# Performance work log

Measured on AMD Instinct MI355X. Metric: run time of the kernel, lower is better.

Reference implementation:

```python
import jax, jax.numpy as jnp
import numpy as np

N_CLASSES = 4
N_FEATURES = 13
N_HIDDEN = 13
N_STEPS = 100
FORGET_BIAS = 1.0


def setup_inputs() -> dict:
    key = jax.random.key(0)
    ks = jax.random.split(key, 10)
    B = 32768
    return {
        "x_input": jax.random.normal(ks[0], (B, N_STEPS, N_FEATURES), dtype=jnp.float32),
        # input projection (tf.random.normal mean=0.5 in original; values irrelevant for correctness test)
        "w_hidden": jax.random.normal(ks[1], (N_FEATURES, N_HIDDEN), dtype=jnp.float32) * 0.5 + 0.5,
        "b_hidden": jax.random.normal(ks[2], (N_HIDDEN,), dtype=jnp.float32) * 0.5 + 0.5,
        # BasicLSTMCell params: kernel [input_dim + hidden, 4*hidden], gate order (i, j, f, o)
        "lstm0_kernel": jax.random.normal(ks[3], (N_HIDDEN + N_HIDDEN, 4 * N_HIDDEN), dtype=jnp.float32) * 0.2,
        "lstm0_bias": jnp.zeros((4 * N_HIDDEN,), dtype=jnp.float32),
        "lstm1_kernel": jax.random.normal(ks[4], (N_HIDDEN + N_HIDDEN, 4 * N_HIDDEN), dtype=jnp.float32) * 0.2,
        "lstm1_bias": jnp.zeros((4 * N_HIDDEN,), dtype=jnp.float32),
        "w_output": jax.random.normal(ks[5], (N_HIDDEN, N_CLASSES), dtype=jnp.float32) * 0.5 + 0.5,
        "b_output": jax.random.normal(ks[6], (N_CLASSES,), dtype=jnp.float32) * 0.5 + 0.5,
    }


def _lstm_cell(x, c, h, kernel, bias):
    # BasicLSTMCell: z = [x; h] @ W + b, split -> i, j, f, o
    z = jnp.concatenate([x, h], axis=-1) @ kernel + bias
    i, j, f, o = jnp.split(z, 4, axis=-1)
    c_new = c * jax.nn.sigmoid(f + FORGET_BIAS) + jax.nn.sigmoid(i) * jnp.tanh(j)
    h_new = jnp.tanh(c_new) * jax.nn.sigmoid(o)
    return c_new, h_new


def reference(x_input, w_hidden, b_hidden, lstm0_kernel, lstm0_bias,
              lstm1_kernel, lstm1_bias, w_output, b_output):
    B = x_input.shape[0]
    # input projection + relu, batched over all timesteps: [B,T,F] -> [T,B,H]
    hidden = jax.nn.relu(jnp.einsum('btf,fh->bth', x_input, w_hidden) + b_hidden)
    hidden = jnp.transpose(hidden, (1, 0, 2))  # [T, B, H]

    zeros = jnp.zeros((B, N_HIDDEN), dtype=x_input.dtype)
    init = (zeros, zeros, zeros, zeros)  # (c0, h0, c1, h1)

    def step(carry, x_t):
        c0, h0, c1, h1 = carry
        c0, h0 = _lstm_cell(x_t, c0, h0, lstm0_kernel, lstm0_bias)
        c1, h1 = _lstm_cell(h0, c1, h1, lstm1_kernel, lstm1_bias)
        return (c0, h0, c1, h1), None

    (c0, h0, c1, h1), _ = jax.lax.scan(step, init, hidden)
    # last output of top LSTM layer -> output projection
    return h1 @ w_output + b_output
```

## Files before the change

### kernel.cpp

```cpp
#include <hip/hip_runtime.h>
#include <cstdint>

typedef __bf16          bf16x8 __attribute__((ext_vector_type(8)));
typedef float           f32x4  __attribute__((ext_vector_type(4)));
typedef unsigned short  u16x8  __attribute__((ext_vector_type(8)));

#define MFMA16(a,b,c) __builtin_amdgcn_mfma_f32_16x16x32_bf16((a),(b),(c),0,0,0)

__device__ __forceinline__ float rcpf(float x) { return __builtin_amdgcn_rcpf(x); }
__device__ __forceinline__ float ex2(float x)  { return __builtin_amdgcn_exp2f(x); }

__device__ __forceinline__ void split2(float v, unsigned short& hi, unsigned short& lo) {
    unsigned u = __builtin_bit_cast(unsigned, v);
    hi = (unsigned short)(u >> 16);
    float rem = v - __builtin_bit_cast(float, u & 0xffff0000u);
    lo = (unsigned short)(__builtin_bit_cast(unsigned, rem) >> 16);
}
__device__ __forceinline__ __bf16 bfbits(unsigned short b) { return __builtin_bit_cast(__bf16, b); }


constexpr float KL = 1.4426950408889634f;

__global__ __launch_bounds__(256, 4)
void lstm_fused(const float* __restrict__ x,
                const float* __restrict__ w_hidden,
                const float* __restrict__ b_hidden,
                const float* __restrict__ k0,
                const float* __restrict__ b0,
                const float* __restrict__ k1,
                const float* __restrict__ b1,
                const float* __restrict__ w_out,
                const float* __restrict__ b_out,
                float* __restrict__ out)
{
    __shared__ __attribute__((aligned(16))) unsigned short xh_s[2][2][2][384];
    __shared__ __attribute__((aligned(16))) unsigned short h0_s[2][2][2][384];
    __shared__ __attribute__((aligned(16))) unsigned short h1_s[2][2][384];

    const int lane = threadIdx.x & 63;
    const int wv   = threadIdx.x >> 6;
    const int grp  = wv >> 1;
    const int role = wv & 1;
    const int col  = lane & 15;
    const int q    = lane >> 4;
    const int qh   = q & 1;
    const int s0   = (blockIdx.x * 2 + grp) * 16;

    {
        unsigned short* a0 = &xh_s[0][0][0][0];
        unsigned short* a1 = &h0_s[0][0][0][0];
        for (int idx = threadIdx.x; idx < 3072; idx += 256) {
            unsigned short v = ((idx % 24) == 13 && ((idx / 384) & 1) == 0)
                             ? (unsigned short)0x3F80 : (unsigned short)0;
            a0[idx] = v; a1[idx] = v;
        }
        unsigned short* a2 = &h1_s[0][0][0];
        for (int idx = threadIdx.x; idx < 1536; idx += 256) {
            unsigned short v = ((idx % 24) == 13 && ((idx / 384) & 1) == 0)
                             ? (unsigned short)0x3F80 : (unsigned short)0;
            a2[idx] = v;
        }
    }

    const float* kp = role ? k1 : k0;
    const float* bb = role ? b1 : b0;
    bf16x8 Kh[4], Kl[4];
    #pragma unroll
    for (int g = 0; g < 4; ++g) {
        bf16x8 hv{}, lv{};
        #pragma unroll
        for (int j = 0; j < 8; ++j) {
            int k = 8 * q + j;
            float w = 0.f;
            if (col < 13) {
                if (k < 13)                 w = kp[k * 52 + 13 * g + col];
                else if (k == 13)           w = bb[13 * g + col] + (g == 2 ? 1.f : 0.f);
                else if (k >= 16 && k < 29) w = kp[(13 + k - 16) * 52 + 13 * g + col];
            }
            unsigned short h_, l_;
            split2(w, h_, l_);
            hv[j] = bfbits(h_); lv[j] = bfbits(l_);
        }
        Kh[g] = hv; Kl[g] = lv;
    }

    bf16x8 Ph{}, Pl{};
    if (role) {
        #pragma unroll
        for (int j = 0; j < 8; ++j) {
            int k = 8 * q + j;
            float w = 0.f;
            if (col < 13) {
                if (k < 13)       w = w_hidden[k * 13 + col];
                else if (k == 13) w = b_hidden[col];
            }
            unsigned short h_, l_;
            split2(w, h_, l_);
            Ph[j] = bfbits(h_); Pl[j] = bfbits(l_);
        }
    }

    const float* xrow = x + (size_t)(s0 + col) * 1300;

    auto elem = [&](float zi, float zj, float zf, float zo, float& c) -> float {
        float a   = ex2(-KL * zi);
        float b   = ex2(-2.f * KL * zj);
        float fe  = ex2(-KL * zf);
        float g   = ex2(-KL * zo);
        float opa = 1.f + a, opb = 1.f + b, opf = 1.f + fe;
        float pab = opa * opb;
        float r1  = rcpf(pab * opf);
        float cn  = fmaf(c, pab, (1.f - b) * opf) * r1;
        c = cn;
        float d   = ex2(-2.f * KL * cn);
        float r2  = rcpf((1.f + d) * (1.f + g));
        return (1.f - d) * r2;
    };

    auto cell = [&](const unsigned short* inH, const unsigned short* hidH,
                    unsigned short* outH, float* cst) {
        const unsigned short* pA = (q < 2) ? inH : hidH;
        bf16x8 ah = __builtin_bit_cast(bf16x8, *(const u16x8*)(pA + col * 24 + 8 * qh));
        bf16x8 al = __builtin_bit_cast(bf16x8, *(const u16x8*)(pA + 384 + col * 24 + 8 * qh));
        f32x4 z0 = {0.f,0.f,0.f,0.f}, z1 = z0, z2 = z0, z3 = z0;
        z0 = MFMA16(ah, Kh[0], z0); z0 = MFMA16(al, Kh[0], z0); z0 = MFMA16(ah, Kl[0], z0);
        z1 = MFMA16(ah, Kh[1], z1); z1 = MFMA16(al, Kh[1], z1); z1 = MFMA16(ah, Kl[1], z1);
        z2 = MFMA16(ah, Kh[2], z2); z2 = MFMA16(al, Kh[2], z2); z2 = MFMA16(ah, Kl[2], z2);
        z3 = MFMA16(ah, Kh[3], z3); z3 = MFMA16(al, Kh[3], z3); z3 = MFMA16(ah, Kl[3], z3);
        #pragma unroll
        for (int r = 0; r < 4; ++r) {
            float hv = elem(z0[r], z1[r], z2[r], z3[r], cst[r]);
            unsigned short hh, hl;
            split2(hv, hh, hl);
            if (col < 13) {
                outH[(4 * q + r) * 24 + col]       = hh;
                outH[384 + (4 * q + r) * 24 + col] = hl;
            }
        }
    };

    auto proj = [&](int t, unsigned short* oH) {
        bf16x8 axh{}, axl{};
        if (q < 2) {
            const float* p = xrow + t * 13;
            #pragma unroll
            for (int j = 0; j < 8; ++j) {
                int k  = 8 * q + j;
                int kk = k > 12 ? 12 : k;
                float v = p[kk];
                if (k > 12) v = 0.f;
                unsigned short h_, l_;
                split2(v, h_, l_);
                axh[j] = bfbits(h_); axl[j] = bfbits(l_);
            }
            if (q == 1) { axh[5] = bfbits(0x3F80); axl[5] = bfbits(0); }
        }
        f32x4 zp = {0.f,0.f,0.f,0.f};
        zp = MFMA16(axh, Ph, zp);
        zp = MFMA16(axl, Ph, zp);
        zp = MFMA16(axh, Pl, zp);
        #pragma unroll
        for (int r = 0; r < 4; ++r) {
            float v = fmaxf(zp[r], 0.f);
            unsigned short hh, hl;
            split2(v, hh, hl);
            if (col < 13) {
                oH[(4 * q + r) * 24 + col]       = hh;
                oH[384 + (4 * q + r) * 24 + col] = hl;
            }
        }
    };

    float cst[4] = {0.f, 0.f, 0.f, 0.f};

    __syncthreads();
    if (role) proj(0, &xh_s[grp][0][0][0]);
    __syncthreads();

    for (int i = 0; i <= 100; ++i) {
        int p = i & 1;
        if (role == 0) {
            if (i < 100)
                cell(&xh_s[grp][p][0][0], &h0_s[grp][p ^ 1][0][0],
                     &h0_s[grp][p][0][0], cst);
        } else {
            if (i >= 1)
                cell(&h0_s[grp][p ^ 1][0][0], &h1_s[grp][0][0],
                     &h1_s[grp][0][0], cst);
            if (i < 99) proj(i + 1, &xh_s[grp][p ^ 1][0][0]);
        }
        __syncthreads();
    }

    if (role) {
        bf16x8 Oh{}, Ol{};
        #pragma unroll
        for (int j = 0; j < 8; ++j) {
            int k = 8 * q + j;
            float w = 0.f;
            if (col < 4) {
                if (k < 13)       w = w_out[k * 4 + col];
                else if (k == 13) w = b_out[col];
            }
            unsigned short h_, l_;
            split2(w, h_, l_);
            Oh[j] = bfbits(h_); Ol[j] = bfbits(l_);
        }
        const unsigned short* pA = &h1_s[grp][0][0];
        bf16x8 ah = __builtin_bit_cast(bf16x8, *(const u16x8*)(pA + col * 24 + 8 * qh));
        bf16x8 al = __builtin_bit_cast(bf16x8, *(const u16x8*)(pA + 384 + col * 24 + 8 * qh));
        f32x4 zf = {0.f,0.f,0.f,0.f};
        zf = MFMA16(ah, Oh, zf);
        zf = MFMA16(al, Oh, zf);
        zf = MFMA16(ah, Ol, zf);
        if (col < 4) {
            #pragma unroll
            for (int r = 0; r < 4; ++r)
                out[(size_t)(s0 + 4 * q + r) * 4 + col] = zf[r];
        }
    }
}

extern "C" void kernel_launch(void* const* d_in, const int* in_sizes, int n_in,
                              void* d_out, int out_size, void* d_ws, size_t ws_size,
                              hipStream_t stream) {
    (void)in_sizes; (void)n_in; (void)d_ws; (void)ws_size; (void)out_size;
    lstm_fused<<<dim3(1024), dim3(256), 0, stream>>>(
        (const float*)d_in[0], (const float*)d_in[1], (const float*)d_in[2],
        (const float*)d_in[3], (const float*)d_in[4], (const float*)d_in[5],
        (const float*)d_in[6], (const float*)d_in[7], (const float*)d_in[8],
        (float*)d_out);
}
```

Before: 370.6 us.

## Shrink blocks to one wave pair and prefetch x two steps ahead

Each block now has two waves instead of four, and the grid doubles to 2048 blocks. Each barrier then synchronises only the two waves that actually depend on each other. The time loop is unrolled by two so the double-buffer indices become constants. Global x loads are issued one step ahead into registers, so they overlap the MFMA and elementwise work instead of stalling the projection. The bf16 hi/lo split of x now uses byte-permute packing, which costs more registers for the prefetch buffers.

```diff
diff --git a/kernel.cpp b/kernel.cpp
--- a/kernel.cpp
+++ b/kernel.cpp
@@ -4,6 +4,7 @@
 typedef __bf16          bf16x8 __attribute__((ext_vector_type(8)));
 typedef float           f32x4  __attribute__((ext_vector_type(4)));
 typedef unsigned short  u16x8  __attribute__((ext_vector_type(8)));
+typedef unsigned int    u32x4  __attribute__((ext_vector_type(4)));
 
 #define MFMA16(a,b,c) __builtin_amdgcn_mfma_f32_16x16x32_bf16((a),(b),(c),0,0,0)
 
@@ -18,10 +19,18 @@
 }
 __device__ __forceinline__ __bf16 bfbits(unsigned short b) { return __builtin_bit_cast(__bf16, b); }
 
+__device__ __forceinline__ unsigned packhi2(float a, float b) {
+    return __builtin_amdgcn_perm(__builtin_bit_cast(unsigned, b),
+                                 __builtin_bit_cast(unsigned, a), 0x07060302u);
+}
+__device__ __forceinline__ float truncrem(float v) {
+    return v - __builtin_bit_cast(float, __builtin_bit_cast(unsigned, v) & 0xffff0000u);
+}
+
 
 constexpr float KL = 1.4426950408889634f;
 
-__global__ __launch_bounds__(256, 4)
+__global__ __launch_bounds__(128, 4)
 void lstm_fused(const float* __restrict__ x,
                 const float* __restrict__ w_hidden,
                 const float* __restrict__ b_hidden,
@@ -33,29 +42,27 @@
                 const float* __restrict__ b_out,
                 float* __restrict__ out)
 {
-    __shared__ __attribute__((aligned(16))) unsigned short xh_s[2][2][2][384];
-    __shared__ __attribute__((aligned(16))) unsigned short h0_s[2][2][2][384];
-    __shared__ __attribute__((aligned(16))) unsigned short h1_s[2][2][384];
+    __shared__ __attribute__((aligned(16))) unsigned short xh_s[2][2][384];
+    __shared__ __attribute__((aligned(16))) unsigned short h0_s[2][2][384];
+    __shared__ __attribute__((aligned(16))) unsigned short h1_s[2][384];
 
     const int lane = threadIdx.x & 63;
-    const int wv   = threadIdx.x >> 6;
-    const int grp  = wv >> 1;
-    const int role = wv & 1;
+    const int role = threadIdx.x >> 6;
     const int col  = lane & 15;
     const int q    = lane >> 4;
     const int qh   = q & 1;
-    const int s0   = (blockIdx.x * 2 + grp) * 16;
+    const int s0   = blockIdx.x * 16;
 
     {
-        unsigned short* a0 = &xh_s[0][0][0][0];
-        unsigned short* a1 = &h0_s[0][0][0][0];
-        for (int idx = threadIdx.x; idx < 3072; idx += 256) {
+        unsigned short* a0 = &xh_s[0][0][0];
+        unsigned short* a1 = &h0_s[0][0][0];
+        for (int idx = threadIdx.x; idx < 1536; idx += 128) {
             unsigned short v = ((idx % 24) == 13 && ((idx / 384) & 1) == 0)
                              ? (unsigned short)0x3F80 : (unsigned short)0;
             a0[idx] = v; a1[idx] = v;
         }
-        unsigned short* a2 = &h1_s[0][0][0];
-        for (int idx = threadIdx.x; idx < 1536; idx += 256) {
+        unsigned short* a2 = &h1_s[0][0];
+        for (int idx = threadIdx.x; idx < 768; idx += 128) {
             unsigned short v = ((idx % 24) == 13 && ((idx / 384) & 1) == 0)
                              ? (unsigned short)0x3F80 : (unsigned short)0;
             a2[idx] = v;
@@ -139,21 +146,38 @@
         }
     };
 
-    auto proj = [&](int t, unsigned short* oH) {
+    auto loadx = [&](int t, float* xv) {
+        if (q < 2) {
+            const float* p = xrow + t * 13 + 8 * q;
+            const int lim = q ? 4 : 7;
+            #pragma unroll
+            for (int j = 0; j < 8; ++j) {
+                int off = j > lim ? lim : j;
+                xv[j] = p[off];
+            }
+        }
+    };
+
+    auto projc = [&](const float* xv, unsigned short* oH) {
         bf16x8 axh{}, axl{};
         if (q < 2) {
-            const float* p = xrow + t * 13;
-            #pragma unroll
-            for (int j = 0; j < 8; ++j) {
-                int k  = 8 * q + j;
-                int kk = k > 12 ? 12 : k;
-                float v = p[kk];
-                if (k > 12) v = 0.f;
-                unsigned short h_, l_;
-                split2(v, h_, l_);
-                axh[j] = bfbits(h_); axl[j] = bfbits(l_);
-            }
-            if (q == 1) { axh[5] = bfbits(0x3F80); axl[5] = bfbits(0); }
+            unsigned hw0 = packhi2(xv[0], xv[1]);
+            unsigned hw1 = packhi2(xv[2], xv[3]);
+            unsigned hw2 = packhi2(xv[4], xv[5]);
+            unsigned hw3 = packhi2(xv[6], xv[7]);
+            unsigned lw0 = packhi2(truncrem(xv[0]), truncrem(xv[1]));
+            unsigned lw1 = packhi2(truncrem(xv[2]), truncrem(xv[3]));
+            unsigned lw2 = packhi2(truncrem(xv[4]), truncrem(xv[5]));
+            unsigned lw3 = packhi2(truncrem(xv[6]), truncrem(xv[7]));
+            if (q == 1) {
+                hw2 = (hw2 & 0xffffu) | 0x3F800000u;
+                lw2 &= 0xffffu;
+                hw3 = 0u; lw3 = 0u;
+            }
+            u32x4 hv = {hw0, hw1, hw2, hw3};
+            u32x4 lv = {lw0, lw1, lw2, lw3};
+            axh = __builtin_bit_cast(bf16x8, hv);
+            axl = __builtin_bit_cast(bf16x8, lv);
         }
         f32x4 zp = {0.f,0.f,0.f,0.f};
         zp = MFMA16(axh, Ph, zp);
@@ -172,27 +196,35 @@
     };
 
     float cst[4] = {0.f, 0.f, 0.f, 0.f};
-
+    float xA[8], xB[8];
+
+    if (role) loadx(0, xA);
     __syncthreads();
-    if (role) proj(0, &xh_s[grp][0][0][0]);
+    if (role) { projc(xA, &xh_s[0][0][0]); loadx(1, xB); }
     __syncthreads();
 
-    for (int i = 0; i <= 100; ++i) {
-        int p = i & 1;
+    for (int i = 0; i < 100; i += 2) {
         if (role == 0) {
-            if (i < 100)
-                cell(&xh_s[grp][p][0][0], &h0_s[grp][p ^ 1][0][0],
-                     &h0_s[grp][p][0][0], cst);
+            cell(&xh_s[0][0][0], &h0_s[1][0][0], &h0_s[0][0][0], cst);
         } else {
-            if (i >= 1)
-                cell(&h0_s[grp][p ^ 1][0][0], &h1_s[grp][0][0],
-                     &h1_s[grp][0][0], cst);
-            if (i < 99) proj(i + 1, &xh_s[grp][p ^ 1][0][0]);
+            if (i < 98) loadx(i + 2, xA);
+            if (i > 0)  cell(&h0_s[1][0][0], &h1_s[0][0], &h1_s[0][0], cst);
+            projc(xB, &xh_s[1][0][0]);
         }
         __syncthreads();
+        if (role == 0) {
+            cell(&xh_s[1][0][0], &h0_s[0][0][0], &h0_s[1][0][0], cst);
+        } else {
+            if (i < 97) loadx(i + 3, xB);
+            cell(&h0_s[0][0][0], &h1_s[0][0], &h1_s[0][0], cst);
+            if (i < 98) projc(xA, &xh_s[0][0][0]);
+        }
+        __syncthreads();
     }
 
     if (role) {
+        cell(&h0_s[1][0][0], &h1_s[0][0], &h1_s[0][0], cst);
+
         bf16x8 Oh{}, Ol{};
         #pragma unroll
         for (int j = 0; j < 8; ++j) {
@@ -206,7 +238,7 @@
             split2(w, h_, l_);
             Oh[j] = bfbits(h_); Ol[j] = bfbits(l_);
         }
-        const unsigned short* pA = &h1_s[grp][0][0];
+        const unsigned short* pA = &h1_s[0][0];
         bf16x8 ah = __builtin_bit_cast(bf16x8, *(const u16x8*)(pA + col * 24 + 8 * qh));
         bf16x8 al = __builtin_bit_cast(bf16x8, *(const u16x8*)(pA + 384 + col * 24 + 8 * qh));
         f32x4 zf = {0.f,0.f,0.f,0.f};
@@ -225,7 +257,7 @@
                               void* d_out, int out_size, void* d_ws, size_t ws_size,
                               hipStream_t stream) {
     (void)in_sizes; (void)n_in; (void)d_ws; (void)ws_size; (void)out_size;
-    lstm_fused<<<dim3(1024), dim3(256), 0, stream>>>(
+    lstm_fused<<<dim3(2048), dim3(128), 0, stream>>>(
         (const float*)d_in[0], (const float*)d_in[1], (const float*)d_in[2],
         (const float*)d_in[3], (const float*)d_in[4], (const float*)d_in[5],
         (const float*)d_in[6], (const float*)d_in[7], (const float*)d_in[8],
```

Measured after the change: 342.0 us. 1.08x faster.
